# Kernel tuning notes

Hardware: AMD Instinct MI355X
Metric: run time of the kernel (lower is better)

The kernel has to match this reference:

```python
import jax, jax.numpy as jnp
import numpy as np

E, S, B, D, F = 8, 2048, 4, 1024, 4096  # experts, seq, batch, d_model, d_ff


def setup_inputs() -> dict:
    key = jax.random.key(0)
    k_x, k_w1, k_w2, k_m = jax.random.split(key, 4)
    scale = 0.02
    x = jax.random.normal(k_x, (S, B, D), dtype=jnp.float32)
    W1 = jax.random.normal(k_w1, (E, D, F), dtype=jnp.float32) * scale
    b1 = jnp.zeros((E, F), dtype=jnp.float32)
    W2 = jax.random.normal(k_w2, (E, F, D), dtype=jnp.float32) * scale
    b2 = jnp.zeros((E, D), dtype=jnp.float32)
    mask = jax.random.randint(k_m, (S, B), 0, E)  # per-token expert id
    return {"x": x, "W1": W1, "b1": b1, "W2": W2, "b2": b2, "mask": mask}


def reference(x, W1, b1, W2, b2, mask):
    # Eval path of ThorFNN: dense all-expert 2-layer FFN, then per-token
    # random expert mask multiply-sum combine. Dropout is identity in eval.
    # h: [E, S, B, F]
    h = jax.nn.relu(jnp.einsum('sbd,edf->esbf', x, W1) + b1[:, None, None, :])
    # out: [E, S, B, D]
    out = jnp.einsum('esbf,efd->esbd', h, W2) + b2[:, None, None, :]
    sel = (mask[None, :, :, None] == jnp.arange(W1.shape[0])[:, None, None, None]).astype(out.dtype)
    return (out * sel).sum(axis=0)  # [S, B, D]
```

## Files before the change

kernel.cpp:

```cpp
#include <hip/hip_runtime.h>
#include <hip/hip_bf16.h>
#include <stdint.h>

#define E_   8
#define S_   2048
#define B_   4
#define D_   1024
#define F_   4096
#define NTOK (S_ * B_)
#define MAXT 72

typedef __attribute__((ext_vector_type(8))) __bf16 bf16x8;
typedef __attribute__((ext_vector_type(4))) float  f32x4;

#define WS_LIST 4096
#define WS_XB   65536
#define WS_W1T  (WS_XB + 16777216)
#define WS_W2T  WS_W1T
#define WS_H    (WS_W1T + 67108864)

__device__ __forceinline__ void gload_lds16(const void* g, void* l) {
    __builtin_amdgcn_global_load_lds(
        (const __attribute__((address_space(1))) void*)g,
        (__attribute__((address_space(3))) void*)l, 16, 0, 0);
}

__global__ void build_lists(const int* __restrict__ mask,
                            int* __restrict__ meta, int* __restrict__ list) {
    __shared__ int cnt[E_], cur[E_];
    int tid = threadIdx.x;
    if (tid < E_) cnt[tid] = 0;
    __syncthreads();
    for (int t = tid; t < NTOK; t += 256) atomicAdd(&cnt[mask[t]], 1);
    __syncthreads();
    if (tid == 0) {
        int acc = 0, nt = 0;
        for (int e = 0; e < E_; ++e) {
            meta[e] = cnt[e];
            meta[8 + e] = acc;
            cur[e] = acc;
            acc += cnt[e];
        }
        for (int e = 0; e < E_; ++e) {
            int mt = (cnt[e] + 127) >> 7;
            for (int m = 0; m < mt; ++m) meta[32 + nt++] = (e << 16) | m;
        }
        meta[16] = nt;
        for (; nt < MAXT; ++nt) meta[32 + nt] = -1;
    }
    __syncthreads();
    for (int t = tid; t < NTOK; t += 256) {
        int e = mask[t];
        int pos = atomicAdd(&cur[e], 1);
        list[pos] = t;
    }
}

__global__ void convert_x_kernel(const float* __restrict__ x,
                                 __hip_bfloat16* __restrict__ xb) {
    size_t i = ((size_t)blockIdx.x * blockDim.x + threadIdx.x) * 4;
    const float4 v = *(const float4*)(x + i);
    union { __hip_bfloat16 h[4]; uint2 u; } o;
    o.h[0] = __float2bfloat16(v.x);
    o.h[1] = __float2bfloat16(v.y);
    o.h[2] = __float2bfloat16(v.z);
    o.h[3] = __float2bfloat16(v.w);
    *(uint2*)(xb + i) = o.u;
}

__global__ void transpose_convert(const float* __restrict__ src,
                                  __hip_bfloat16* __restrict__ dst,
                                  int R, int C) {
    size_t off = (size_t)blockIdx.z * R * C;
    const float* s = src + off;
    __hip_bfloat16* d = dst + off;
    int r0 = blockIdx.y * 128, c0 = blockIdx.x * 128;
    int t = threadIdx.x;
    int rb = t >> 4, cb = t & 15;
    const float* sp = s + (size_t)(r0 + 8 * rb) * C + c0 + 8 * cb;
    float v[8][8];
#pragma unroll
    for (int j = 0; j < 8; ++j) {
        *(float4*)&v[j][0] = *(const float4*)(sp + (size_t)j * C);
        *(float4*)&v[j][4] = *(const float4*)(sp + (size_t)j * C + 4);
    }
    __hip_bfloat16* dp = d + (size_t)(c0 + 8 * cb) * R + r0 + 8 * rb;
#pragma unroll
    for (int i = 0; i < 8; ++i) {
        union { __hip_bfloat16 h[8]; uint4 u; } o;
#pragma unroll
        for (int j = 0; j < 8; ++j) o.h[j] = __float2bfloat16(v[j][i]);
        *(uint4*)(dp + (size_t)i * R) = o.u;
    }
}

template <int KDIM, int NDIM, int LAYER>
__global__ __launch_bounds__(256, 4) void gemm_kernel(
    const uint8_t* __restrict__ Abase,
    const uint8_t* __restrict__ Wt,
    const float* __restrict__ bias,
    const int* __restrict__ meta, const int* __restrict__ list,
    __hip_bfloat16* __restrict__ Hout, float* __restrict__ Oout) {
    constexpr int NT = NDIM / 128;
    const int nblk = MAXT * NT;
    int orig = blockIdx.x;
    int q = nblk >> 3, r = nblk & 7;
    int xcd = orig & 7, idx = orig >> 3;
    int swz = (xcd < r ? xcd * (q + 1) : r * (q + 1) + (xcd - r) * q) + idx;
    int te = meta[32 + swz / NT];
    if (te < 0) return;
    const int e = te >> 16, mt = te & 0xffff;
    const int cnt = meta[e], bse = meta[8 + e];
    const int n0 = (swz % NT) * 128;
    const int tid = threadIdx.x, wv = tid >> 6, l = tid & 63;
    const int wr = wv >> 1, wc = wv & 1;

    __shared__ __align__(16) uint8_t smem[2][16384];

    const uint8_t* WtE = Wt + (size_t)e * NDIM * KDIM * 2;

    size_t agoff[2], bgoff[2];
#pragma unroll
    for (int p = 0; p < 2; ++p) {
        int rrow = p * 64 + wv * 16 + (l >> 2);
        int grow = mt * 128 + rrow;
        int pidx = bse + (grow < cnt ? grow : cnt - 1);
        size_t arow = (LAYER == 1) ? (size_t)list[pidx] : (size_t)pidx;
        size_t chunk = (size_t)(((l & 3) ^ ((l >> 3) & 3)) * 16);
        agoff[p] = arow * (KDIM * 2) + chunk;
        bgoff[p] = (size_t)(n0 + rrow) * (KDIM * 2) + chunk;
    }

    f32x4 acc[4][4] = {};

    auto stage = [&](int buf, int kt) {
        uint8_t* As = &smem[buf][0];
        uint8_t* Bs = &smem[buf][8192];
        size_t kb = (size_t)kt * 64;
#pragma unroll
        for (int p = 0; p < 2; ++p) {
            gload_lds16(Abase + agoff[p] + kb, As + (p * 64 + wv * 16) * 64);
            gload_lds16(WtE + bgoff[p] + kb, Bs + (p * 64 + wv * 16) * 64);
        }
    };

    auto compute = [&](int buf) {
        const uint8_t* As = &smem[buf][0];
        const uint8_t* Bs = &smem[buf][8192];
        bf16x8 a[4], b[4];
#pragma unroll
        for (int mi = 0; mi < 4; ++mi) {
            int row = wr * 64 + mi * 16 + (l & 15);
            a[mi] = *(const bf16x8*)(As + row * 64 +
                                     (((l >> 4) ^ ((row >> 1) & 3)) << 4));
        }
#pragma unroll
        for (int ni = 0; ni < 4; ++ni) {
            int row = wc * 64 + ni * 16 + (l & 15);
            b[ni] = *(const bf16x8*)(Bs + row * 64 +
                                     (((l >> 4) ^ ((row >> 1) & 3)) << 4));
        }
#pragma unroll
        for (int mi = 0; mi < 4; ++mi)
#pragma unroll
            for (int ni = 0; ni < 4; ++ni)
                acc[mi][ni] = __builtin_amdgcn_mfma_f32_16x16x32_bf16(
                    a[mi], b[ni], acc[mi][ni], 0, 0, 0);
    };

    const int KT = KDIM / 32;
    stage(0, 0);
    __syncthreads();
    int cur = 0;
    for (int kt = 0; kt < KT - 1; ++kt) {
        stage(cur ^ 1, kt + 1);
        compute(cur);
        __syncthreads();
        cur ^= 1;
    }
    compute(cur);

#pragma unroll
    for (int mi = 0; mi < 4; ++mi) {
#pragma unroll
        for (int i = 0; i < 4; ++i) {
            int rl = wr * 64 + mi * 16 + (l >> 4) * 4 + i;
            int grow = mt * 128 + rl;
            if (grow < cnt) {
#pragma unroll
                for (int ni = 0; ni < 4; ++ni) {
                    int col = n0 + wc * 64 + ni * 16 + (l & 15);
                    float v = acc[mi][ni][i] + bias[(size_t)e * NDIM + col];
                    if (LAYER == 1) {
                        v = fmaxf(v, 0.f);
                        Hout[(size_t)(bse + grow) * NDIM + col] = __float2bfloat16(v);
                    } else {
                        int tok = list[bse + grow];
                        Oout[(size_t)tok * NDIM + col] = v;
                    }
                }
            }
        }
    }
}

extern "C" void kernel_launch(void* const* d_in, const int* in_sizes, int n_in,
                              void* d_out, int out_size, void* d_ws, size_t ws_size,
                              hipStream_t stream) {
    const float* x  = (const float*)d_in[0];
    const float* W1 = (const float*)d_in[1];
    const float* b1 = (const float*)d_in[2];
    const float* W2 = (const float*)d_in[3];
    const float* b2 = (const float*)d_in[4];
    const int* mask = (const int*)d_in[5];
    float* out = (float*)d_out;

    uint8_t* ws = (uint8_t*)d_ws;
    int* meta = (int*)ws;
    int* list = (int*)(ws + WS_LIST);
    __hip_bfloat16* xb  = (__hip_bfloat16*)(ws + WS_XB);
    __hip_bfloat16* w1t = (__hip_bfloat16*)(ws + WS_W1T);
    __hip_bfloat16* w2t = (__hip_bfloat16*)(ws + WS_W2T);
    __hip_bfloat16* H   = (__hip_bfloat16*)(ws + WS_H);

    build_lists<<<1, 256, 0, stream>>>(mask, meta, list);
    convert_x_kernel<<<NTOK * D_ / 4 / 256, 256, 0, stream>>>(x, xb);
    transpose_convert<<<dim3(F_ / 128, D_ / 128, E_), 256, 0, stream>>>(W1, w1t, D_, F_);
    gemm_kernel<D_, F_, 1><<<MAXT * (F_ / 128), 256, 0, stream>>>(
        (const uint8_t*)xb, (const uint8_t*)w1t, b1, meta, list, H, nullptr);
    transpose_convert<<<dim3(D_ / 128, F_ / 128, E_), 256, 0, stream>>>(W2, w2t, F_, D_);
    gemm_kernel<F_, D_, 2><<<MAXT * (D_ / 128), 256, 0, stream>>>(
        (const uint8_t*)H, (const uint8_t*)w2t, b2, meta, list, nullptr, out);
}
```

Baseline: 568.7 us.

## Use 256x128 tiles with 8 waves and triple-buffered K=64 LDS pipeline

Replaces the 128x128, 4-wave, double-buffered grouped GEMM with a 512-thread kernel that computes 256-row by 128-column tiles. It uses a three-stage LDS ring of 48KB per stage, K-steps of 64 with an 8-chunk XOR swizzle, explicit vmcnt waits, and raw barriers. MFMA issue priority is raised with s_setprio. The goal is more reuse of each weight tile across tokens and better hiding of global-to-LDS latency. The cost is one block per CU, fewer tiles to spread across CUs, and more padding waste in each expert's last tile.

```diff
diff --git a/kernel.cpp b/kernel.cpp
--- a/kernel.cpp
+++ b/kernel.cpp
@@ -8,7 +8,7 @@
 #define D_   1024
 #define F_   4096
 #define NTOK (S_ * B_)
-#define MAXT 72
+#define MAXT 40
 
 typedef __attribute__((ext_vector_type(8))) __bf16 bf16x8;
 typedef __attribute__((ext_vector_type(4))) float  f32x4;
@@ -42,7 +42,7 @@
             acc += cnt[e];
         }
         for (int e = 0; e < E_; ++e) {
-            int mt = (cnt[e] + 127) >> 7;
+            int mt = (cnt[e] + 255) >> 8;
             for (int m = 0; m < mt; ++m) meta[32 + nt++] = (e << 16) | m;
         }
         meta[16] = nt;
@@ -95,12 +95,13 @@
 }
 
 template <int KDIM, int NDIM, int LAYER>
-__global__ __launch_bounds__(256, 4) void gemm_kernel(
+__global__ __launch_bounds__(512, 1) void gemm8_kernel(
     const uint8_t* __restrict__ Abase,
     const uint8_t* __restrict__ Wt,
     const float* __restrict__ bias,
     const int* __restrict__ meta, const int* __restrict__ list,
     __hip_bfloat16* __restrict__ Hout, float* __restrict__ Oout) {
+    extern __shared__ __align__(16) uint8_t smem[];
     constexpr int NT = NDIM / 128;
     const int nblk = MAXT * NT;
     int orig = blockIdx.x;
@@ -113,83 +114,91 @@
     const int cnt = meta[e], bse = meta[8 + e];
     const int n0 = (swz % NT) * 128;
     const int tid = threadIdx.x, wv = tid >> 6, l = tid & 63;
-    const int wr = wv >> 1, wc = wv & 1;
-
-    __shared__ __align__(16) uint8_t smem[2][16384];
+    const int wr = wv >> 1, wcn = wv & 1;
 
     const uint8_t* WtE = Wt + (size_t)e * NDIM * KDIM * 2;
 
-    size_t agoff[2], bgoff[2];
-#pragma unroll
-    for (int p = 0; p < 2; ++p) {
-        int rrow = p * 64 + wv * 16 + (l >> 2);
-        int grow = mt * 128 + rrow;
+    const int srcchunk = ((l & 7) ^ ((l >> 3) & 7)) * 16;
+    size_t agoff[4], bgoff[2];
+#pragma unroll
+    for (int p = 0; p < 4; ++p) {
+        int rrow = p * 64 + wv * 8 + (l >> 3);
+        int grow = mt * 256 + rrow;
         int pidx = bse + (grow < cnt ? grow : cnt - 1);
         size_t arow = (LAYER == 1) ? (size_t)list[pidx] : (size_t)pidx;
-        size_t chunk = (size_t)(((l & 3) ^ ((l >> 3) & 3)) * 16);
-        agoff[p] = arow * (KDIM * 2) + chunk;
-        bgoff[p] = (size_t)(n0 + rrow) * (KDIM * 2) + chunk;
+        agoff[p] = arow * (KDIM * 2) + srcchunk;
+    }
+#pragma unroll
+    for (int p = 0; p < 2; ++p) {
+        int rrow = p * 64 + wv * 8 + (l >> 3);
+        bgoff[p] = (size_t)(n0 + rrow) * (KDIM * 2) + srcchunk;
     }
 
     f32x4 acc[4][4] = {};
 
-    auto stage = [&](int buf, int kt) {
-        uint8_t* As = &smem[buf][0];
-        uint8_t* Bs = &smem[buf][8192];
-        size_t kb = (size_t)kt * 64;
-#pragma unroll
-        for (int p = 0; p < 2; ++p) {
-            gload_lds16(Abase + agoff[p] + kb, As + (p * 64 + wv * 16) * 64);
-            gload_lds16(WtE + bgoff[p] + kb, Bs + (p * 64 + wv * 16) * 64);
-        }
+    auto stage = [&](int kt) {
+        uint8_t* As = smem + (kt % 3) * 49152;
+        uint8_t* Bs = As + 32768;
+        size_t kb = (size_t)kt * 128;
+#pragma unroll
+        for (int p = 0; p < 4; ++p)
+            gload_lds16(Abase + agoff[p] + kb, As + p * 8192 + wv * 1024);
+#pragma unroll
+        for (int p = 0; p < 2; ++p)
+            gload_lds16(WtE + bgoff[p] + kb, Bs + p * 8192 + wv * 1024);
     };
 
-    auto compute = [&](int buf) {
-        const uint8_t* As = &smem[buf][0];
-        const uint8_t* Bs = &smem[buf][8192];
+    auto subphase = [&](const uint8_t* As, const uint8_t* Bs, int ks) {
         bf16x8 a[4], b[4];
 #pragma unroll
         for (int mi = 0; mi < 4; ++mi) {
             int row = wr * 64 + mi * 16 + (l & 15);
-            a[mi] = *(const bf16x8*)(As + row * 64 +
-                                     (((l >> 4) ^ ((row >> 1) & 3)) << 4));
+            int ch = (ks * 4 + (l >> 4)) ^ (row & 7);
+            a[mi] = *(const bf16x8*)(As + row * 128 + ch * 16);
         }
 #pragma unroll
         for (int ni = 0; ni < 4; ++ni) {
-            int row = wc * 64 + ni * 16 + (l & 15);
-            b[ni] = *(const bf16x8*)(Bs + row * 64 +
-                                     (((l >> 4) ^ ((row >> 1) & 3)) << 4));
-        }
+            int row = wcn * 64 + ni * 16 + (l & 15);
+            int ch = (ks * 4 + (l >> 4)) ^ (row & 7);
+            b[ni] = *(const bf16x8*)(Bs + row * 128 + ch * 16);
+        }
+        __builtin_amdgcn_s_setprio(1);
 #pragma unroll
         for (int mi = 0; mi < 4; ++mi)
 #pragma unroll
             for (int ni = 0; ni < 4; ++ni)
                 acc[mi][ni] = __builtin_amdgcn_mfma_f32_16x16x32_bf16(
                     a[mi], b[ni], acc[mi][ni], 0, 0, 0);
+        __builtin_amdgcn_s_setprio(0);
     };
 
-    const int KT = KDIM / 32;
-    stage(0, 0);
-    __syncthreads();
-    int cur = 0;
-    for (int kt = 0; kt < KT - 1; ++kt) {
-        stage(cur ^ 1, kt + 1);
-        compute(cur);
-        __syncthreads();
-        cur ^= 1;
-    }
-    compute(cur);
+    const int KT = KDIM / 64;
+    stage(0); stage(1); stage(2);
+    for (int t = 0; t < KT; ++t) {
+        if (t + 2 < KT)      asm volatile("s_waitcnt vmcnt(12)" ::: "memory");
+        else if (t + 1 < KT) asm volatile("s_waitcnt vmcnt(6)" ::: "memory");
+        else                 asm volatile("s_waitcnt vmcnt(0)" ::: "memory");
+        __builtin_amdgcn_s_barrier();
+        __builtin_amdgcn_sched_barrier(0);
+        const uint8_t* As = smem + (t % 3) * 49152;
+        const uint8_t* Bs = As + 32768;
+        subphase(As, Bs, 0);
+        __builtin_amdgcn_s_barrier();
+        subphase(As, Bs, 1);
+        __builtin_amdgcn_s_barrier();
+        if (t + 3 < KT) stage(t + 3);
+    }
 
 #pragma unroll
     for (int mi = 0; mi < 4; ++mi) {
 #pragma unroll
         for (int i = 0; i < 4; ++i) {
             int rl = wr * 64 + mi * 16 + (l >> 4) * 4 + i;
-            int grow = mt * 128 + rl;
+            int grow = mt * 256 + rl;
             if (grow < cnt) {
 #pragma unroll
                 for (int ni = 0; ni < 4; ++ni) {
-                    int col = n0 + wc * 64 + ni * 16 + (l & 15);
+                    int col = n0 + wcn * 64 + ni * 16 + (l & 15);
                     float v = acc[mi][ni][i] + bias[(size_t)e * NDIM + col];
                     if (LAYER == 1) {
                         v = fmaxf(v, 0.f);
@@ -223,12 +232,18 @@
     __hip_bfloat16* w2t = (__hip_bfloat16*)(ws + WS_W2T);
     __hip_bfloat16* H   = (__hip_bfloat16*)(ws + WS_H);
 
+    const int LDS_BYTES = 3 * 49152;
+    hipFuncSetAttribute(reinterpret_cast<const void*>(&gemm8_kernel<D_, F_, 1>),
+                        hipFuncAttributeMaxDynamicSharedMemorySize, LDS_BYTES);
+    hipFuncSetAttribute(reinterpret_cast<const void*>(&gemm8_kernel<F_, D_, 2>),
+                        hipFuncAttributeMaxDynamicSharedMemorySize, LDS_BYTES);
+
     build_lists<<<1, 256, 0, stream>>>(mask, meta, list);
     convert_x_kernel<<<NTOK * D_ / 4 / 256, 256, 0, stream>>>(x, xb);
     transpose_convert<<<dim3(F_ / 128, D_ / 128, E_), 256, 0, stream>>>(W1, w1t, D_, F_);
-    gemm_kernel<D_, F_, 1><<<MAXT * (F_ / 128), 256, 0, stream>>>(
+    gemm8_kernel<D_, F_, 1><<<MAXT * (F_ / 128), 512, LDS_BYTES, stream>>>(
         (const uint8_t*)xb, (const uint8_t*)w1t, b1, meta, list, H, nullptr);
     transpose_convert<<<dim3(D_ / 128, F_ / 128, E_), 256, 0, stream>>>(W2, w2t, F_, D_);
-    gemm_kernel<F_, D_, 2><<<MAXT * (D_ / 128), 256, 0, stream>>>(
+    gemm8_kernel<F_, D_, 2><<<MAXT * (D_ / 128), 512, LDS_BYTES, stream>>>(
         (const uint8_t*)H, (const uint8_t*)w2t, b2, meta, list, nullptr, out);
 }
```

After: 612.8 us. +7.7%, slower.
